# Optimization experiments

Hardware: AMD Instinct MI355X
Metric: run time of the kernel (lower is better)

The kernel has to match this reference:

```python
import jax, jax.numpy as jnp
import numpy as np

B, S, D, H = 2, 4096, 512, 8
HD = D // H  # head_dim = 64


def setup_inputs() -> dict:
    key = jax.random.key(0)
    ks = jax.random.split(key, 13)
    scale = 1.0 / np.sqrt(D)
    inp = {
        "query": jax.random.normal(ks[0], (B, S, D), dtype=jnp.float32),
        "key": jax.random.normal(ks[1], (B, S, D), dtype=jnp.float32),
        "value": jax.random.normal(ks[2], (B, S, D), dtype=jnp.float32),
        "mask": jax.random.randint(ks[3], (B, S, S), 0, 2, dtype=jnp.int32),
        "Wq": jax.random.normal(ks[4], (D, D), dtype=jnp.float32) * scale,
        "bq": jnp.zeros((D,), dtype=jnp.float32),
        "Wk": jax.random.normal(ks[5], (D, D), dtype=jnp.float32) * scale,
        "bk": jnp.zeros((D,), dtype=jnp.float32),
        "Wv": jax.random.normal(ks[6], (D, D), dtype=jnp.float32) * scale,
        "bv": jnp.zeros((D,), dtype=jnp.float32),
        "Wo": jax.random.normal(ks[7], (D, D), dtype=jnp.float32) * scale,
        "bo": jnp.zeros((D,), dtype=jnp.float32),
    }
    return inp


def reference(query, key, value, mask, Wq, bq, Wk, bk, Wv, bv, Wo, bo):
    # Linear projections (torch Linear: x @ W.T + b), split heads: [B,H,S,HD]
    def split_heads(x):
        return x.reshape(B, S, H, HD).transpose(0, 2, 1, 3)

    q = split_heads(query @ Wq.T + bq)
    k = split_heads(key @ Wk.T + bk)
    v = split_heads(value @ Wv.T + bv)

    # NOTE: original module applies NO 1/sqrt(head_dim) scaling.
    scores = jnp.einsum("bhqd,bhkd->bhqk", q, k)  # [B,H,S,S]
    scores = jnp.where(mask[:, None, :, :] == 0, jnp.float32(-1e9), scores)
    probs = jax.nn.softmax(scores, axis=-1)
    attn = jnp.einsum("bhqk,bhkd->bhqd", probs, v)  # [B,H,S,HD]
    attn = attn.transpose(0, 2, 1, 3).reshape(B, S, D)
    return attn @ Wo.T + bo
```

## Files before the change

### kernel.cpp

```cpp
#include <hip/hip_runtime.h>
#include <hip/hip_bf16.h>
#include <cstddef>
#include <cstdint>


#define S_LEN 4096
#define DMODEL 512
#define NHEAD 8
#define HDIM 64
#define NWORDS (S_LEN / 64)

typedef __bf16 bf16x8 __attribute__((ext_vector_type(8)));
typedef _Float16 f16x8 __attribute__((ext_vector_type(8)));
typedef _Float16 f16x2 __attribute__((ext_vector_type(2)));
typedef float f32x4 __attribute__((ext_vector_type(4)));
typedef float f32x16 __attribute__((ext_vector_type(16)));
typedef unsigned int u32x4 __attribute__((ext_vector_type(4)));
typedef unsigned short u16x4 __attribute__((ext_vector_type(4)));
typedef unsigned short u16x8 __attribute__((ext_vector_type(8)));

__device__ __forceinline__ unsigned short f2bf(float x) {
  return __builtin_bit_cast(unsigned short, (__bf16)x);
}
__device__ __forceinline__ float bf2f(unsigned short h) {
  union { unsigned u; float f; } v; v.u = ((unsigned)h) << 16; return v.f;
}
__device__ __forceinline__ float fast_exp2(float x) {
#if __has_builtin(__builtin_amdgcn_exp2f)
  return __builtin_amdgcn_exp2f(x);
#else
  return __expf(x * 0.69314718056f);
#endif
}
__device__ __forceinline__ float max3f(float a, float b, float c) {
  return fmaxf(fmaxf(a, b), c);
}
__device__ __forceinline__ int swzi(int row, int col) {
  return row * 64 + ((col & 7) | ((((col >> 3) ^ row) & 7) << 3));
}

__global__ __launch_bounds__(256) void pack_mask(
    const int* __restrict__ mask, unsigned long long* __restrict__ bits, int nwords)
{
  int gw = (blockIdx.x * blockDim.x + threadIdx.x) >> 6;
  int lane = threadIdx.x & 63;
  int nw = (gridDim.x * blockDim.x) >> 6;
  for (int w = gw; w < nwords; w += nw) {
    int v = mask[(size_t)w * 64 + lane];
    unsigned long long b = __ballot(v != 0);
    if (lane == 0) bits[w] = b;
  }
}

__global__ __launch_bounds__(256) void conv_hilo(
    const float* __restrict__ x, unsigned short* __restrict__ h,
    unsigned short* __restrict__ l, int n4)
{
  int i = blockIdx.x * 256 + threadIdx.x;
  int stride = gridDim.x * 256;
  for (; i < n4; i += stride) {
    float4 f = ((const float4*)x)[i];
    float ff[4] = {f.x, f.y, f.z, f.w};
    u16x4 hh, ll;
    #pragma unroll
    for (int j = 0; j < 4; ++j) {
      unsigned short hb = f2bf(ff[j]);
      hh[j] = hb;
      ll[j] = f2bf(ff[j] - bf2f(hb));
    }
    ((u16x4*)h)[i] = hh;
    ((u16x4*)l)[i] = ll;
  }
}

__global__ __launch_bounds__(256) void conv_w4(
    const float* __restrict__ w0, const float* __restrict__ w1,
    const float* __restrict__ w2, const float* __restrict__ w3,
    unsigned short* __restrict__ out)
{
  const float* src = (blockIdx.y == 0) ? w0 : (blockIdx.y == 1) ? w1 : (blockIdx.y == 2) ? w2 : w3;
  unsigned short* h = out + (size_t)blockIdx.y * 2 * 262144;
  unsigned short* l = h + 262144;
  int i = blockIdx.x * 256 + threadIdx.x;
  float4 f = ((const float4*)src)[i];
  float ff[4] = {f.x, f.y, f.z, f.w};
  u16x4 hh, ll;
  #pragma unroll
  for (int j = 0; j < 4; ++j) {
    unsigned short hb = f2bf(ff[j]);
    hh[j] = hb;
    ll[j] = f2bf(ff[j] - bf2f(hb));
  }
  ((u16x4*)h)[i] = hh;
  ((u16x4*)l)[i] = ll;
}

template <int MODE>
__global__ __launch_bounds__(256) void gemm_pre(
    const unsigned short* __restrict__ xh, const unsigned short* __restrict__ xl,
    const unsigned short* __restrict__ wh, const unsigned short* __restrict__ wl,
    const float* __restrict__ bias, void* __restrict__ out0, void* __restrict__ out1,
    float oscale)
{
  __shared__ __align__(16) unsigned short SMEM[24576];
  unsigned short* Xh = SMEM;
  unsigned short* Xl = SMEM + 8192;
  unsigned short* Wh = SMEM + 16384;
  unsigned short* Wl = SMEM + 20480;

  const int t = threadIdx.x;
  const int lane = t & 63;
  const int w = t >> 6;
  const int c = lane & 15;
  const int g = lane >> 4;
  const int row0 = blockIdx.x * 128;
  const int col0 = blockIdx.y * 64;

  f32x4 acc[2][4];
  #pragma unroll
  for (int mi = 0; mi < 2; ++mi)
    #pragma unroll
    for (int n = 0; n < 4; ++n) acc[mi][n] = (f32x4){0.f, 0.f, 0.f, 0.f};

  u16x8 pxh[4], pxl[4], pwh[2], pwl[2];
  auto issue = [&](int k0) {
    #pragma unroll
    for (int i = 0; i < 4; ++i) {
      int id = i * 256 + t;
      int r = id >> 3, ch = id & 7;
      size_t off = (size_t)(row0 + r) * DMODEL + k0 + ch * 8;
      pxh[i] = *(const u16x8*)(xh + off);
      pxl[i] = *(const u16x8*)(xl + off);
    }
    #pragma unroll
    for (int i = 0; i < 2; ++i) {
      int id = i * 256 + t;
      int r = id >> 3, ch = id & 7;
      size_t off = (size_t)(col0 + r) * DMODEL + k0 + ch * 8;
      pwh[i] = *(const u16x8*)(wh + off);
      pwl[i] = *(const u16x8*)(wl + off);
    }
  };
  auto commit = [&]() {
    #pragma unroll
    for (int i = 0; i < 4; ++i) {
      int id = i * 256 + t;
      int r = id >> 3, ch = id & 7;
      int dst = r * 64 + (((ch ^ r) & 7) << 3);
      *(u16x8*)&Xh[dst] = pxh[i];
      *(u16x8*)&Xl[dst] = pxl[i];
    }
    #pragma unroll
    for (int i = 0; i < 2; ++i) {
      int id = i * 256 + t;
      int r = id >> 3, ch = id & 7;
      int dst = r * 64 + (((ch ^ r) & 7) << 3);
      *(u16x8*)&Wh[dst] = pwh[i];
      *(u16x8*)&Wl[dst] = pwl[i];
    }
  };

  issue(0);
  commit();
  __syncthreads();

  for (int k0 = 0; k0 < DMODEL; k0 += 64) {
    const bool more = (k0 + 64) < DMODEL;
    if (more) issue(k0 + 64);

    #pragma unroll
    for (int kk = 0; kk < 2; ++kk) {
      bf16x8 ah[2], al[2], bh_[4], bl_[4];
      #pragma unroll
      for (int mi = 0; mi < 2; ++mi) {
        int r = w * 32 + mi * 16 + c;
        ah[mi] = __builtin_bit_cast(bf16x8, *(const u16x8*)&Xh[swzi(r, (kk * 4 + g) * 8)]);
        al[mi] = __builtin_bit_cast(bf16x8, *(const u16x8*)&Xl[swzi(r, (kk * 4 + g) * 8)]);
      }
      #pragma unroll
      for (int n = 0; n < 4; ++n) {
        int r = n * 16 + c;
        bh_[n] = __builtin_bit_cast(bf16x8, *(const u16x8*)&Wh[swzi(r, (kk * 4 + g) * 8)]);
        bl_[n] = __builtin_bit_cast(bf16x8, *(const u16x8*)&Wl[swzi(r, (kk * 4 + g) * 8)]);
      }
      #pragma unroll
      for (int mi = 0; mi < 2; ++mi)
        #pragma unroll
        for (int n = 0; n < 4; ++n) {
          acc[mi][n] = __builtin_amdgcn_mfma_f32_16x16x32_bf16(ah[mi], bh_[n], acc[mi][n], 0, 0, 0);
          acc[mi][n] = __builtin_amdgcn_mfma_f32_16x16x32_bf16(al[mi], bh_[n], acc[mi][n], 0, 0, 0);
          acc[mi][n] = __builtin_amdgcn_mfma_f32_16x16x32_bf16(ah[mi], bl_[n], acc[mi][n], 0, 0, 0);
        }
    }
    __syncthreads();
    if (more) {
      commit();
      __syncthreads();
    }
  }

  if (MODE == 0) {
    unsigned short* Yf = (unsigned short*)out0;
    #pragma unroll
    for (int mi = 0; mi < 2; ++mi)
      #pragma unroll
      for (int n = 0; n < 4; ++n)
        #pragma unroll
        for (int j = 0; j < 4; ++j) {
          int rr = row0 + w * 32 + mi * 16 + g * 4 + j;
          int oo = col0 + n * 16 + c;
          float val = (acc[mi][n][j] + bias[oo]) * oscale;
          int bb = rr >> 12, ss = rr & (S_LEN - 1), h2 = oo >> 6, hd = oo & 63;
          size_t idx = (((size_t)(bb * NHEAD + h2)) * S_LEN + ss) * HDIM + hd;
          Yf[idx] = __builtin_bit_cast(unsigned short, (_Float16)val);
        }
  } else if (MODE == 1) {
    float* Y = (float*)out0;
    #pragma unroll
    for (int mi = 0; mi < 2; ++mi)
      #pragma unroll
      for (int n = 0; n < 4; ++n)
        #pragma unroll
        for (int j = 0; j < 4; ++j) {
          int rr = row0 + w * 32 + mi * 16 + g * 4 + j;
          int oo = col0 + n * 16 + c;
          Y[(size_t)rr * DMODEL + oo] = acc[mi][n][j] + bias[oo];
        }
  } else {
    unsigned short* Ts = SMEM;
    #pragma unroll
    for (int mi = 0; mi < 2; ++mi)
      #pragma unroll
      for (int n = 0; n < 4; ++n)
        #pragma unroll
        for (int j = 0; j < 4; ++j) {
          int r = w * 32 + mi * 16 + g * 4 + j;
          int o = n * 16 + c;
          Ts[r * 68 + o] = __builtin_bit_cast(unsigned short, (_Float16)(acc[mi][n][j] + bias[col0 + o]));
        }
    __syncthreads();
    unsigned short* vt = (unsigned short*)out0;
    int bb = row0 >> 12, sbase = row0 & (S_LEN - 1), h2 = col0 >> 6;
    int d = t >> 2, s0 = (t & 3) * 32;
    size_t obase = ((size_t)((bb * NHEAD + h2) * HDIM + d)) * S_LEN + sbase + s0;
    #pragma unroll
    for (int i = 0; i < 4; ++i) {
      u16x8 v;
      #pragma unroll
      for (int jj = 0; jj < 8; ++jj) v[jj] = Ts[(s0 + i * 8 + jj) * 68 + d];
      *(u16x8*)(vt + obase + i * 8) = v;
    }
  }
}

__global__ __launch_bounds__(256) void attn32(
    const unsigned short* __restrict__ qf, const unsigned short* __restrict__ kf,
    const unsigned short* __restrict__ vt, const unsigned long long* __restrict__ mbits,
    unsigned short* __restrict__ Oh, unsigned short* __restrict__ Ol)
{
  __shared__ __align__(16) unsigned short LDS[2][2][4096];

  const int t = threadIdx.x;
  const int lane = t & 63;
  const int w = t >> 6;
  const int pair = w >> 1;
  const int chunk = w & 1;
  const int c31 = lane & 31;
  const int hi = lane >> 5;

  const int nwg = gridDim.x;
  const int bid = blockIdx.x;
  const int lin = (bid & 7) * (nwg >> 3) + (bid >> 3);
  const int qi = lin & 63;
  const int bh = lin >> 6;
  const int q0 = qi * 64;
  const int b = bh >> 3, h = bh & 7;
  const int qrow = q0 + pair * 32 + c31;

  const unsigned short* Qp = qf + ((size_t)bh * S_LEN + qrow) * HDIM;
  f16x8 qfr[4];
  #pragma unroll
  for (int s = 0; s < 4; ++s)
    qfr[s] = __builtin_bit_cast(f16x8, *(const u16x8*)(Qp + 16 * s + 8 * hi));

  const unsigned short* Kb = kf + (size_t)bh * S_LEN * HDIM;
  const unsigned short* Vbt = vt + (size_t)bh * HDIM * S_LEN;
  const unsigned long long* mptr = mbits + (size_t)(b * S_LEN + qrow) * NWORDS;

  const int sr0 = t >> 3, sch = t & 7;
  const int sr1 = sr0 + 32;
  const int dst0 = sr0 * 64 + (((sch ^ sr0) & 7) << 3);
  const int dst1 = sr1 * 64 + (((sch ^ sr1) & 7) << 3);
  u16x8 pkk[2], pkv[2];
  auto issue = [&](int k0) {
    pkk[0] = *(const u16x8*)(Kb + (size_t)(k0 + sr0) * HDIM + sch * 8);
    pkk[1] = *(const u16x8*)(Kb + (size_t)(k0 + sr1) * HDIM + sch * 8);
    pkv[0] = *(const u16x8*)(Vbt + (size_t)sr0 * S_LEN + k0 + sch * 8);
    pkv[1] = *(const u16x8*)(Vbt + (size_t)sr1 * S_LEN + k0 + sch * 8);
  };
  auto commit = [&](int buf) {
    *(u16x8*)&LDS[buf][0][dst0] = pkk[0];
    *(u16x8*)&LDS[buf][0][dst1] = pkk[1];
    *(u16x8*)&LDS[buf][1][dst0] = pkv[0];
    *(u16x8*)&LDS[buf][1][dst1] = pkv[1];
  };

  f32x16 oacc0, oacc1;
  #pragma unroll
  for (int r = 0; r < 16; ++r) { oacc0[r] = 0.f; oacc1[r] = 0.f; }
  float mrow = -INFINITY, lrow = 0.f;

  unsigned long long m64 = mptr[0], m64n = 0;

  issue(0);
  commit(0);
  __syncthreads();

  int cur = 0;
  for (int kt = 0; kt < S_LEN / 64; ++kt) {
    const bool more = kt < (S_LEN / 64 - 1);
    if (more) {
      issue((kt + 1) * 64);
      m64n = mptr[kt + 1];
    }
    const unsigned short* K_ = &LDS[cur][0][0];
    const unsigned short* Vt_ = &LDS[cur][1][0];

    f32x16 p;
    #pragma unroll
    for (int r = 0; r < 16; ++r) p[r] = 0.f;
    __builtin_amdgcn_s_setprio(1);
    #pragma unroll
    for (int s = 0; s < 4; ++s) {
      int idx = swzi(chunk * 32 + c31, 16 * s + 8 * hi);
      f16x8 kfr = __builtin_bit_cast(f16x8, *(const u16x8*)&K_[idx]);
      p = __builtin_amdgcn_mfma_f32_32x32x16_f16(kfr, qfr[s], p, 0, 0, 0);
    }
    __builtin_amdgcn_s_setprio(0);

    unsigned half = chunk ? (unsigned)(m64 >> 32) : (unsigned)m64;
    unsigned hs = half >> (hi * 4);
    #pragma unroll
    for (int r = 0; r < 16; ++r) {
      int bs = (r & 3) + 8 * (r >> 2);
      p[r] = ((hs >> bs) & 1u) ? p[r] : -1.0e9f;
    }

    float t0 = max3f(p[0], p[1], p[2]);
    float t1 = max3f(p[3], p[4], p[5]);
    float t2 = max3f(p[6], p[7], p[8]);
    float t3 = max3f(p[9], p[10], p[11]);
    float t4 = max3f(p[12], p[13], p[14]);
    float mx = fmaxf(max3f(t0, t1, t2), max3f(t3, t4, p[15]));
    mx = fmaxf(mx, __shfl_xor(mx, 32, 64));

    float mn, scl;
    if (__all(mx <= mrow + 11.54f)) {
      mn = mrow;
      scl = 1.0f;
    } else {
      mn = fmaxf(mrow, mx);
      scl = fast_exp2(mrow - mn);
      mrow = mn;
      oacc0 *= scl;
      oacc1 *= scl;
    }
    #pragma unroll
    for (int r = 0; r < 16; ++r) p[r] = fast_exp2(p[r] - mn);
    float s0_ = (p[0] + p[1]) + (p[2] + p[3]);
    float s1_ = (p[4] + p[5]) + (p[6] + p[7]);
    float s2_ = (p[8] + p[9]) + (p[10] + p[11]);
    float s3_ = (p[12] + p[13]) + (p[14] + p[15]);
    float ps = (s0_ + s1_) + (s2_ + s3_);
    ps += __shfl_xor(ps, 32, 64);
    lrow = lrow * scl + ps;

    unsigned W[4][2];
    #pragma unroll
    for (int rq = 0; rq < 4; ++rq) {
      W[rq][0] = __builtin_bit_cast(unsigned, __builtin_amdgcn_cvt_pkrtz(p[4 * rq + 0], p[4 * rq + 1]));
      W[rq][1] = __builtin_bit_cast(unsigned, __builtin_amdgcn_cvt_pkrtz(p[4 * rq + 2], p[4 * rq + 3]));
    }
    f16x8 pf[2];
    #pragma unroll
    for (int s2 = 0; s2 < 2; ++s2) {
      unsigned keep0 = hi ? W[2 * s2 + 1][0] : W[2 * s2][0];
      unsigned keep1 = hi ? W[2 * s2 + 1][1] : W[2 * s2][1];
      unsigned send0 = hi ? W[2 * s2][0] : W[2 * s2 + 1][0];
      unsigned send1 = hi ? W[2 * s2][1] : W[2 * s2 + 1][1];
      unsigned recv0 = (unsigned)__shfl_xor((int)send0, 32, 64);
      unsigned recv1 = (unsigned)__shfl_xor((int)send1, 32, 64);
      u32x4 fw;
      fw[0] = hi ? recv0 : keep0;
      fw[1] = hi ? recv1 : keep1;
      fw[2] = hi ? keep0 : recv0;
      fw[3] = hi ? keep1 : recv1;
      pf[s2] = __builtin_bit_cast(f16x8, fw);
    }

    __builtin_amdgcn_s_setprio(1);
    #pragma unroll
    for (int s2 = 0; s2 < 2; ++s2) {
      int col = chunk * 32 + 16 * s2 + 8 * hi;
      f16x8 vf0 = __builtin_bit_cast(f16x8, *(const u16x8*)&Vt_[swzi(c31, col)]);
      f16x8 vf1 = __builtin_bit_cast(f16x8, *(const u16x8*)&Vt_[swzi(32 + c31, col)]);
      oacc0 = __builtin_amdgcn_mfma_f32_32x32x16_f16(vf0, pf[s2], oacc0, 0, 0, 0);
      oacc1 = __builtin_amdgcn_mfma_f32_32x32x16_f16(vf1, pf[s2], oacc1, 0, 0, 0);
    }
    __builtin_amdgcn_s_setprio(0);

    if (more) {
      m64 = m64n;
      commit(cur ^ 1);
    }
    __syncthreads();
    cur ^= 1;
  }

  float* mb = (float*)&LDS[0][0][0];
  const int mi = ((pair * 2 + hi) * 32 + c31) * 36;
  if (chunk == 1) {
    #pragma unroll
    for (int q4 = 0; q4 < 4; ++q4) {
      *(f32x4*)&mb[mi + q4 * 4]      = (f32x4){oacc0[q4 * 4], oacc0[q4 * 4 + 1], oacc0[q4 * 4 + 2], oacc0[q4 * 4 + 3]};
      *(f32x4*)&mb[mi + 16 + q4 * 4] = (f32x4){oacc1[q4 * 4], oacc1[q4 * 4 + 1], oacc1[q4 * 4 + 2], oacc1[q4 * 4 + 3]};
    }
    mb[mi + 32] = mrow;
    mb[mi + 33] = lrow;
  }
  __syncthreads();
  if (chunk == 0) {
    float m1 = mb[mi + 32], l1 = mb[mi + 33];
    float mS = fmaxf(mrow, m1);
    float f0 = fast_exp2(mrow - mS), f1 = fast_exp2(m1 - mS);
    float lS = lrow * f0 + l1 * f1;
    float inv = 1.0f / lS;
    size_t obase = ((size_t)b * S_LEN + qrow) * DMODEL + h * HDIM;
    #pragma unroll
    for (int c2 = 0; c2 < 2; ++c2) {
      #pragma unroll
      for (int rq = 0; rq < 4; ++rq) {
        u16x4 hv, lv;
        #pragma unroll
        for (int rb = 0; rb < 4; ++rb) {
          int reg = 4 * rq + rb;
          float o0 = (c2 == 0) ? oacc0[reg] : oacc1[reg];
          float o1 = mb[mi + c2 * 16 + reg];
          float val = (o0 * f0 + o1 * f1) * inv;
          unsigned short hb = f2bf(val);
          hv[rb] = hb;
          lv[rb] = f2bf(val - bf2f(hb));
        }
        int dbase = 32 * c2 + 8 * rq + 4 * hi;
        *(u16x4*)(Oh + obase + dbase) = hv;
        *(u16x4*)(Ol + obase + dbase) = lv;
      }
    }
  }
}

extern "C" void kernel_launch(void* const* d_in, const int* in_sizes, int n_in,
                              void* d_out, int out_size, void* d_ws, size_t ws_size,
                              hipStream_t stream) {
  const float* query = (const float*)d_in[0];
  const float* key   = (const float*)d_in[1];
  const float* value = (const float*)d_in[2];
  const int*   mask  = (const int*)  d_in[3];
  const float* Wq = (const float*)d_in[4];
  const float* bq = (const float*)d_in[5];
  const float* Wk = (const float*)d_in[6];
  const float* bk = (const float*)d_in[7];
  const float* Wv = (const float*)d_in[8];
  const float* bv = (const float*)d_in[9];
  const float* Wo = (const float*)d_in[10];
  const float* bo = (const float*)d_in[11];
  float* out = (float*)d_out;

  const size_t PER = (size_t)2 * S_LEN * DMODEL;
  const size_t WSZ = (size_t)DMODEL * DMODEL;

  unsigned short* p = (unsigned short*)d_ws;
  unsigned short* wbuf = p;
  unsigned short* xh = p + 8 * WSZ;
  unsigned short* xl = xh + PER;
  unsigned short* qfb = xl + PER;
  unsigned short* kfb = qfb + PER;
  unsigned short* vtb = kfb + PER;

  unsigned short* wqh = wbuf + 0 * 2 * WSZ, *wql = wqh + WSZ;
  unsigned short* wkh = wbuf + 1 * 2 * WSZ, *wkl = wkh + WSZ;
  unsigned short* wvh = wbuf + 2 * 2 * WSZ, *wvl = wvh + WSZ;
  unsigned short* woh = wbuf + 3 * 2 * WSZ, *wol = woh + WSZ;

  unsigned long long* bits = (unsigned long long*)d_out;
  pack_mask<<<2048, 256, 0, stream>>>(mask, bits, 2 * S_LEN * NWORDS);
  conv_w4<<<dim3(256, 4), 256, 0, stream>>>(Wq, Wk, Wv, Wo, wbuf);

  dim3 gg(2 * S_LEN / 128, DMODEL / 64);
  const int N4 = (int)(PER / 4);

  conv_hilo<<<2048, 256, 0, stream>>>(query, xh, xl, N4);
  gemm_pre<0><<<gg, 256, 0, stream>>>(xh, xl, wqh, wql, bq, qfb, nullptr, 1.44269504f);

  conv_hilo<<<2048, 256, 0, stream>>>(key, xh, xl, N4);
  gemm_pre<0><<<gg, 256, 0, stream>>>(xh, xl, wkh, wkl, bk, kfb, nullptr, 1.0f);

  conv_hilo<<<2048, 256, 0, stream>>>(value, xh, xl, N4);
  gemm_pre<2><<<gg, 256, 0, stream>>>(xh, xl, wvh, wvl, bv, vtb, nullptr, 1.0f);

  attn32<<<1024, 256, 0, stream>>>(qfb, kfb, vtb, bits, xh, xl);

  gemm_pre<1><<<gg, 256, 0, stream>>>(xh, xl, woh, wol, bo, out, nullptr, 1.0f);
}
```

Measured before the change: 274.7 us.

## Fuse preprocessing kernels, drop split-precision for V and output projections, tweak softmax ops

```diff
diff --git a/kernel.cpp b/kernel.cpp
--- a/kernel.cpp
+++ b/kernel.cpp
@@ -12,9 +12,9 @@
 
 typedef __bf16 bf16x8 __attribute__((ext_vector_type(8)));
 typedef _Float16 f16x8 __attribute__((ext_vector_type(8)));
-typedef _Float16 f16x2 __attribute__((ext_vector_type(2)));
 typedef float f32x4 __attribute__((ext_vector_type(4)));
 typedef float f32x16 __attribute__((ext_vector_type(16)));
+typedef int i32x2 __attribute__((ext_vector_type(2)));
 typedef unsigned int u32x4 __attribute__((ext_vector_type(4)));
 typedef unsigned short u16x4 __attribute__((ext_vector_type(4)));
 typedef unsigned short u16x8 __attribute__((ext_vector_type(8)));
@@ -35,73 +35,112 @@
 __device__ __forceinline__ float max3f(float a, float b, float c) {
   return fmaxf(fmaxf(a, b), c);
 }
+__device__ __forceinline__ int bit_mask(unsigned hs, int bs) {
+#if __has_builtin(__builtin_amdgcn_sbfe)
+  return __builtin_amdgcn_sbfe((int)hs, bs, 1);
+#else
+  return ((int)(hs << (31 - bs))) >> 31;
+#endif
+}
+__device__ __forceinline__ float mask_blend(float x, int msk) {
+  const int NEG = __builtin_bit_cast(int, -1.0e9f);
+  int xi = __builtin_bit_cast(int, x);
+  return __builtin_bit_cast(float, (xi & msk) | (NEG & ~msk));
+}
+__device__ __forceinline__ void pl_swap(int& a, int& b) {
+#if __has_builtin(__builtin_amdgcn_permlane32_swap)
+  i32x2 r = __builtin_amdgcn_permlane32_swap(a, b, false, false);
+  a = r[0]; b = r[1];
+#else
+  asm volatile("v_permlane32_swap_b32 %0, %1" : "+v"(a), "+v"(b));
+#endif
+}
+__device__ __forceinline__ float xhalf_max(float x) {
+  int a = __builtin_bit_cast(int, x), b = a;
+  pl_swap(a, b);
+  return fmaxf(__builtin_bit_cast(float, a), __builtin_bit_cast(float, b));
+}
+__device__ __forceinline__ float xhalf_sum(float x) {
+  int a = __builtin_bit_cast(int, x), b = a;
+  pl_swap(a, b);
+  return __builtin_bit_cast(float, a) + __builtin_bit_cast(float, b);
+}
 __device__ __forceinline__ int swzi(int row, int col) {
   return row * 64 + ((col & 7) | ((((col >> 3) ^ row) & 7) << 3));
 }
 
-__global__ __launch_bounds__(256) void pack_mask(
-    const int* __restrict__ mask, unsigned long long* __restrict__ bits, int nwords)
-{
-  int gw = (blockIdx.x * blockDim.x + threadIdx.x) >> 6;
-  int lane = threadIdx.x & 63;
-  int nw = (gridDim.x * blockDim.x) >> 6;
-  for (int w = gw; w < nwords; w += nw) {
-    int v = mask[(size_t)w * 64 + lane];
-    unsigned long long b = __ballot(v != 0);
-    if (lane == 0) bits[w] = b;
-  }
-}
-
-__global__ __launch_bounds__(256) void conv_hilo(
-    const float* __restrict__ x, unsigned short* __restrict__ h,
-    unsigned short* __restrict__ l, int n4)
-{
-  int i = blockIdx.x * 256 + threadIdx.x;
-  int stride = gridDim.x * 256;
-  for (; i < n4; i += stride) {
-    float4 f = ((const float4*)x)[i];
-    float ff[4] = {f.x, f.y, f.z, f.w};
-    u16x4 hh, ll;
-    #pragma unroll
-    for (int j = 0; j < 4; ++j) {
-      unsigned short hb = f2bf(ff[j]);
-      hh[j] = hb;
-      ll[j] = f2bf(ff[j] - bf2f(hb));
-    }
-    ((u16x4*)h)[i] = hh;
-    ((u16x4*)l)[i] = ll;
-  }
-}
-
-__global__ __launch_bounds__(256) void conv_w4(
+__global__ __launch_bounds__(256) void prep(
+    const float* __restrict__ query, const float* __restrict__ key,
+    const float* __restrict__ value,
     const float* __restrict__ w0, const float* __restrict__ w1,
     const float* __restrict__ w2, const float* __restrict__ w3,
-    unsigned short* __restrict__ out)
+    const int* __restrict__ mask,
+    unsigned short* __restrict__ qh, unsigned short* __restrict__ ql,
+    unsigned short* __restrict__ kh, unsigned short* __restrict__ kl,
+    unsigned short* __restrict__ vh, unsigned short* __restrict__ vl,
+    unsigned short* __restrict__ wbuf, unsigned long long* __restrict__ bits)
 {
-  const float* src = (blockIdx.y == 0) ? w0 : (blockIdx.y == 1) ? w1 : (blockIdx.y == 2) ? w2 : w3;
-  unsigned short* h = out + (size_t)blockIdx.y * 2 * 262144;
-  unsigned short* l = h + 262144;
-  int i = blockIdx.x * 256 + threadIdx.x;
-  float4 f = ((const float4*)src)[i];
-  float ff[4] = {f.x, f.y, f.z, f.w};
-  u16x4 hh, ll;
-  #pragma unroll
-  for (int j = 0; j < 4; ++j) {
-    unsigned short hb = f2bf(ff[j]);
-    hh[j] = hb;
-    ll[j] = f2bf(ff[j] - bf2f(hb));
+  const int task = blockIdx.y;
+  const int tid = blockIdx.x * 256 + threadIdx.x;
+  const int nthr = gridDim.x * 256;
+
+  if (task < 3) {
+    const float* x = (task == 0) ? query : (task == 1) ? key : value;
+    unsigned short* h = (task == 0) ? qh : (task == 1) ? kh : vh;
+    unsigned short* l = (task == 0) ? ql : (task == 1) ? kl : vl;
+    const int n4 = (int)((size_t)2 * S_LEN * DMODEL / 4);
+    for (int i = tid; i < n4; i += nthr) {
+      float4 f = ((const float4*)x)[i];
+      float ff[4] = {f.x, f.y, f.z, f.w};
+      u16x4 hh, ll;
+      #pragma unroll
+      for (int j = 0; j < 4; ++j) {
+        unsigned short hb = f2bf(ff[j]);
+        hh[j] = hb;
+        ll[j] = f2bf(ff[j] - bf2f(hb));
+      }
+      ((u16x4*)h)[i] = hh;
+      ((u16x4*)l)[i] = ll;
+    }
+  } else if (task == 3) {
+    const int per = 65536;
+    for (int i = tid; i < 4 * per; i += nthr) {
+      int wsel = i >> 16, idx = i & (per - 1);
+      const float* src = (wsel == 0) ? w0 : (wsel == 1) ? w1 : (wsel == 2) ? w2 : w3;
+      unsigned short* h = wbuf + (size_t)wsel * 2 * 262144;
+      unsigned short* l = h + 262144;
+      float4 f = ((const float4*)src)[idx];
+      float ff[4] = {f.x, f.y, f.z, f.w};
+      u16x4 hh, ll;
+      #pragma unroll
+      for (int j = 0; j < 4; ++j) {
+        unsigned short hb = f2bf(ff[j]);
+        hh[j] = hb;
+        ll[j] = f2bf(ff[j] - bf2f(hb));
+      }
+      ((u16x4*)h)[idx] = hh;
+      ((u16x4*)l)[idx] = ll;
+    }
+  } else {
+    const int nwords = 2 * S_LEN * NWORDS;
+    int gw = tid >> 6;
+    int lane = threadIdx.x & 63;
+    int nw = nthr >> 6;
+    for (int w = gw; w < nwords; w += nw) {
+      int v = mask[(size_t)w * 64 + lane];
+      unsigned long long bm = __ballot(v != 0);
+      if (lane == 0) bits[w] = bm;
+    }
   }
-  ((u16x4*)h)[i] = hh;
-  ((u16x4*)l)[i] = ll;
 }
 
 template <int MODE>
 __global__ __launch_bounds__(256) void gemm_pre(
     const unsigned short* __restrict__ xh, const unsigned short* __restrict__ xl,
     const unsigned short* __restrict__ wh, const unsigned short* __restrict__ wl,
-    const float* __restrict__ bias, void* __restrict__ out0, void* __restrict__ out1,
-    float oscale)
+    const float* __restrict__ bias, void* __restrict__ out0, float oscale)
 {
+  constexpr bool TRI = (MODE == 0);
   __shared__ __align__(16) unsigned short SMEM[24576];
   unsigned short* Xh = SMEM;
   unsigned short* Xl = SMEM + 8192;
@@ -130,7 +169,7 @@
       int r = id >> 3, ch = id & 7;
       size_t off = (size_t)(row0 + r) * DMODEL + k0 + ch * 8;
       pxh[i] = *(const u16x8*)(xh + off);
-      pxl[i] = *(const u16x8*)(xl + off);
+      if (TRI) pxl[i] = *(const u16x8*)(xl + off);
     }
     #pragma unroll
     for (int i = 0; i < 2; ++i) {
@@ -138,7 +177,7 @@
       int r = id >> 3, ch = id & 7;
       size_t off = (size_t)(col0 + r) * DMODEL + k0 + ch * 8;
       pwh[i] = *(const u16x8*)(wh + off);
-      pwl[i] = *(const u16x8*)(wl + off);
+      if (TRI) pwl[i] = *(const u16x8*)(wl + off);
     }
   };
   auto commit = [&]() {
@@ -148,7 +187,7 @@
       int r = id >> 3, ch = id & 7;
       int dst = r * 64 + (((ch ^ r) & 7) << 3);
       *(u16x8*)&Xh[dst] = pxh[i];
-      *(u16x8*)&Xl[dst] = pxl[i];
+      if (TRI) *(u16x8*)&Xl[dst] = pxl[i];
     }
     #pragma unroll
     for (int i = 0; i < 2; ++i) {
@@ -156,7 +195,7 @@
       int r = id >> 3, ch = id & 7;
       int dst = r * 64 + (((ch ^ r) & 7) << 3);
       *(u16x8*)&Wh[dst] = pwh[i];
-      *(u16x8*)&Wl[dst] = pwl[i];
+      if (TRI) *(u16x8*)&Wl[dst] = pwl[i];
     }
   };
 
@@ -175,21 +214,23 @@
       for (int mi = 0; mi < 2; ++mi) {
         int r = w * 32 + mi * 16 + c;
         ah[mi] = __builtin_bit_cast(bf16x8, *(const u16x8*)&Xh[swzi(r, (kk * 4 + g) * 8)]);
-        al[mi] = __builtin_bit_cast(bf16x8, *(const u16x8*)&Xl[swzi(r, (kk * 4 + g) * 8)]);
+        if (TRI) al[mi] = __builtin_bit_cast(bf16x8, *(const u16x8*)&Xl[swzi(r, (kk * 4 + g) * 8)]);
       }
       #pragma unroll
       for (int n = 0; n < 4; ++n) {
         int r = n * 16 + c;
         bh_[n] = __builtin_bit_cast(bf16x8, *(const u16x8*)&Wh[swzi(r, (kk * 4 + g) * 8)]);
-        bl_[n] = __builtin_bit_cast(bf16x8, *(const u16x8*)&Wl[swzi(r, (kk * 4 + g) * 8)]);
+        if (TRI) bl_[n] = __builtin_bit_cast(bf16x8, *(const u16x8*)&Wl[swzi(r, (kk * 4 + g) * 8)]);
       }
       #pragma unroll
       for (int mi = 0; mi < 2; ++mi)
         #pragma unroll
         for (int n = 0; n < 4; ++n) {
           acc[mi][n] = __builtin_amdgcn_mfma_f32_16x16x32_bf16(ah[mi], bh_[n], acc[mi][n], 0, 0, 0);
-          acc[mi][n] = __builtin_amdgcn_mfma_f32_16x16x32_bf16(al[mi], bh_[n], acc[mi][n], 0, 0, 0);
-          acc[mi][n] = __builtin_amdgcn_mfma_f32_16x16x32_bf16(ah[mi], bl_[n], acc[mi][n], 0, 0, 0);
+          if (TRI) {
+            acc[mi][n] = __builtin_amdgcn_mfma_f32_16x16x32_bf16(al[mi], bh_[n], acc[mi][n], 0, 0, 0);
+            acc[mi][n] = __builtin_amdgcn_mfma_f32_16x16x32_bf16(ah[mi], bl_[n], acc[mi][n], 0, 0, 0);
+          }
         }
     }
     __syncthreads();
@@ -228,6 +269,7 @@
         }
   } else {
     unsigned short* Ts = SMEM;
+    __syncthreads();
     #pragma unroll
     for (int mi = 0; mi < 2; ++mi)
       #pragma unroll
@@ -256,7 +298,7 @@
 __global__ __launch_bounds__(256) void attn32(
     const unsigned short* __restrict__ qf, const unsigned short* __restrict__ kf,
     const unsigned short* __restrict__ vt, const unsigned long long* __restrict__ mbits,
-    unsigned short* __restrict__ Oh, unsigned short* __restrict__ Ol)
+    unsigned short* __restrict__ Ob)
 {
   __shared__ __align__(16) unsigned short LDS[2][2][4096];
 
@@ -308,6 +350,7 @@
   f32x16 oacc0, oacc1;
   #pragma unroll
   for (int r = 0; r < 16; ++r) { oacc0[r] = 0.f; oacc1[r] = 0.f; }
+  const f32x16 fzero = oacc0;
   float mrow = -INFINITY, lrow = 0.f;
 
   unsigned long long m64 = mptr[0], m64n = 0;
@@ -327,11 +370,14 @@
     const unsigned short* Vt_ = &LDS[cur][1][0];
 
     f32x16 p;
-    #pragma unroll
-    for (int r = 0; r < 16; ++r) p[r] = 0.f;
     __builtin_amdgcn_s_setprio(1);
-    #pragma unroll
-    for (int s = 0; s < 4; ++s) {
+    {
+      int idx = swzi(chunk * 32 + c31, 8 * hi);
+      f16x8 kfr = __builtin_bit_cast(f16x8, *(const u16x8*)&K_[idx]);
+      p = __builtin_amdgcn_mfma_f32_32x32x16_f16(kfr, qfr[0], fzero, 0, 0, 0);
+    }
+    #pragma unroll
+    for (int s = 1; s < 4; ++s) {
       int idx = swzi(chunk * 32 + c31, 16 * s + 8 * hi);
       f16x8 kfr = __builtin_bit_cast(f16x8, *(const u16x8*)&K_[idx]);
       p = __builtin_amdgcn_mfma_f32_32x32x16_f16(kfr, qfr[s], p, 0, 0, 0);
@@ -343,7 +389,7 @@
     #pragma unroll
     for (int r = 0; r < 16; ++r) {
       int bs = (r & 3) + 8 * (r >> 2);
-      p[r] = ((hs >> bs) & 1u) ? p[r] : -1.0e9f;
+      p[r] = mask_blend(p[r], bit_mask(hs, bs));
     }
 
     float t0 = max3f(p[0], p[1], p[2]);
@@ -352,7 +398,7 @@
     float t3 = max3f(p[9], p[10], p[11]);
     float t4 = max3f(p[12], p[13], p[14]);
     float mx = fmaxf(max3f(t0, t1, t2), max3f(t3, t4, p[15]));
-    mx = fmaxf(mx, __shfl_xor(mx, 32, 64));
+    mx = xhalf_max(mx);
 
     float mn, scl;
     if (__all(mx <= mrow + 11.54f)) {
@@ -365,14 +411,15 @@
       oacc0 *= scl;
       oacc1 *= scl;
     }
+
     #pragma unroll
     for (int r = 0; r < 16; ++r) p[r] = fast_exp2(p[r] - mn);
+
     float s0_ = (p[0] + p[1]) + (p[2] + p[3]);
     float s1_ = (p[4] + p[5]) + (p[6] + p[7]);
     float s2_ = (p[8] + p[9]) + (p[10] + p[11]);
     float s3_ = (p[12] + p[13]) + (p[14] + p[15]);
-    float ps = (s0_ + s1_) + (s2_ + s3_);
-    ps += __shfl_xor(ps, 32, 64);
+    float ps = xhalf_sum((s0_ + s1_) + (s2_ + s3_));
     lrow = lrow * scl + ps;
 
     unsigned W[4][2];
@@ -440,20 +487,15 @@
     for (int c2 = 0; c2 < 2; ++c2) {
       #pragma unroll
       for (int rq = 0; rq < 4; ++rq) {
-        u16x4 hv, lv;
+        u16x4 hv;
         #pragma unroll
         for (int rb = 0; rb < 4; ++rb) {
           int reg = 4 * rq + rb;
           float o0 = (c2 == 0) ? oacc0[reg] : oacc1[reg];
           float o1 = mb[mi + c2 * 16 + reg];
-          float val = (o0 * f0 + o1 * f1) * inv;
-          unsigned short hb = f2bf(val);
-          hv[rb] = hb;
-          lv[rb] = f2bf(val - bf2f(hb));
+          hv[rb] = f2bf((o0 * f0 + o1 * f1) * inv);
         }
-        int dbase = 32 * c2 + 8 * rq + 4 * hi;
-        *(u16x4*)(Oh + obase + dbase) = hv;
-        *(u16x4*)(Ol + obase + dbase) = lv;
+        *(u16x4*)(Ob + obase + 32 * c2 + 8 * rq + 4 * hi) = hv;
       }
     }
   }
@@ -483,32 +525,30 @@
   unsigned short* wbuf = p;
   unsigned short* xh = p + 8 * WSZ;
   unsigned short* xl = xh + PER;
-  unsigned short* qfb = xl + PER;
+  unsigned short* yh = xl + PER;
+  unsigned short* yl = yh + PER;
+  unsigned short* zh = yl + PER;
+  unsigned short* zl = zh + PER;
+  unsigned short* qfb = zl + PER;
   unsigned short* kfb = qfb + PER;
   unsigned short* vtb = kfb + PER;
 
   unsigned short* wqh = wbuf + 0 * 2 * WSZ, *wql = wqh + WSZ;
   unsigned short* wkh = wbuf + 1 * 2 * WSZ, *wkl = wkh + WSZ;
   unsigned short* wvh = wbuf + 2 * 2 * WSZ, *wvl = wvh + WSZ;
-  unsigned short* woh = wbuf + 3 * 2 * WSZ, *wol = woh + WSZ;
+  unsigned short* woh = wbuf + 3 * 2 * WSZ;
 
   unsigned long long* bits = (unsigned long long*)d_out;
-  pack_mask<<<2048, 256, 0, stream>>>(mask, bits, 2 * S_LEN * NWORDS);
-  conv_w4<<<dim3(256, 4), 256, 0, stream>>>(Wq, Wk, Wv, Wo, wbuf);
+
+  prep<<<dim3(2048, 5), 256, 0, stream>>>(query, key, value, Wq, Wk, Wv, Wo, mask,
+                                          xh, xl, yh, yl, zh, zl, wbuf, bits);
 
   dim3 gg(2 * S_LEN / 128, DMODEL / 64);
-  const int N4 = (int)(PER / 4);
-
-  conv_hilo<<<2048, 256, 0, stream>>>(query, xh, xl, N4);
-  gemm_pre<0><<<gg, 256, 0, stream>>>(xh, xl, wqh, wql, bq, qfb, nullptr, 1.44269504f);
-
-  conv_hilo<<<2048, 256, 0, stream>>>(key, xh, xl, N4);
-  gemm_pre<0><<<gg, 256, 0, stream>>>(xh, xl, wkh, wkl, bk, kfb, nullptr, 1.0f);
-
-  conv_hilo<<<2048, 256, 0, stream>>>(value, xh, xl, N4);
-  gemm_pre<2><<<gg, 256, 0, stream>>>(xh, xl, wvh, wvl, bv, vtb, nullptr, 1.0f);
-
-  attn32<<<1024, 256, 0, stream>>>(qfb, kfb, vtb, bits, xh, xl);
-
-  gemm_pre<1><<<gg, 256, 0, stream>>>(xh, xl, woh, wol, bo, out, nullptr, 1.0f);
-}
+  gemm_pre<0><<<gg, 256, 0, stream>>>(xh, xl, wqh, wql, bq, qfb, 1.44269504f);
+  gemm_pre<0><<<gg, 256, 0, stream>>>(yh, yl, wkh, wkl, bk, kfb, 1.0f);
+  gemm_pre<2><<<gg, 256, 0, stream>>>(zh, zl, wvh, wvl, bv, vtb, 1.0f);
+
+  attn32<<<1024, 256, 0, stream>>>(qfb, kfb, vtb, bits, xh);
+
+  gemm_pre<1><<<gg, 256, 0, stream>>>(xh, nullptr, woh, nullptr, bo, out, 1.0f);
+}
```

New measurement: 257.1 us. 1.07x faster.
